# Performance work log

Hardware: AMD Instinct MI355X
Metric: run time of the kernel (lower is better)

The kernel has to match this reference:

```python
import jax, jax.numpy as jnp
import numpy as np

D_MODEL = 1024
N_HEADS = 16
HEAD_DIM = D_MODEL // N_HEADS
B, S = 2, 2048


def setup_inputs() -> dict:
    key = jax.random.key(0)
    ks = jax.random.split(key, 10)
    q = jax.random.normal(ks[0], (B, S, D_MODEL), dtype=jnp.float32)
    k = jax.random.normal(ks[1], (B, S, D_MODEL), dtype=jnp.float32)
    v = jax.random.normal(ks[2], (B, S, D_MODEL), dtype=jnp.float32)
    # causal mask: 1 where attention is forbidden (upper triangle), 0 elsewhere
    mask = jnp.triu(jnp.ones((S, S), dtype=jnp.float32), k=1)[None, None, :, :]
    scale = 0.02
    Wk = jax.random.normal(ks[3], (D_MODEL, D_MODEL), dtype=jnp.float32) * scale
    bk = jnp.zeros((D_MODEL,), dtype=jnp.float32)
    Wv = jax.random.normal(ks[4], (D_MODEL, D_MODEL), dtype=jnp.float32) * scale
    bv = jnp.zeros((D_MODEL,), dtype=jnp.float32)
    Wo = jax.random.normal(ks[5], (D_MODEL, D_MODEL), dtype=jnp.float32) * scale
    bo = jnp.zeros((D_MODEL,), dtype=jnp.float32)
    return {"query": q, "key": k, "value": v, "mask": mask,
            "Wk": Wk, "bk": bk, "Wv": Wv, "bv": bv, "Wo": Wo, "bo": bo}


def reference(query, key, value, mask, Wk, bk, Wv, bv, Wo, bo):
    b, s, d = query.shape
    h, dh = N_HEADS, HEAD_DIM

    def split(x):  # [b, s, d] -> [b, h, s, dh]
        return x.reshape(b, -1, h, dh).transpose(0, 2, 1, 3)

    # NOTE: faithful to source bug — query is projected with weights_key.
    q = split(query @ Wk.T + bk)
    k = split(key @ Wk.T + bk)
    v = split(value @ Wv.T + bv)

    inv_sqrt_dh = jnp.float32(1.0 / np.sqrt(dh))
    scores = jnp.einsum('bhqd,bhkd->bhqk', q, k) * inv_sqrt_dh
    scores = scores + mask * jnp.float32(-1e9)
    w = jax.nn.softmax(scores, axis=-1)           # [b, h, s, s]
    ctx = jnp.einsum('bhqk,bhkd->bhqd', w, v)     # [b, h, s, dh]
    concat = ctx.transpose(0, 2, 1, 3).reshape(b, -1, d)
    out = concat @ Wo.T + bo
    return (out, w)
```

## Files before the change

kernel.cpp:

```cpp
#include <hip/hip_runtime.h>
#include <stdint.h>

#define BB 2
#define SS 2048
#define DD 1024
#define HH 16
#define DH 64
#define MM 4096

typedef unsigned short u16;
typedef __attribute__((ext_vector_type(8))) __bf16 bf16x8;
typedef __attribute__((ext_vector_type(4))) float f32x4;

__device__ __forceinline__ u16 f2bf(float f) {
    union { float f; unsigned int u; } x; x.f = f;
    unsigned int u = x.u;
    return (u16)((u + 0x7fffu + ((u >> 16) & 1u)) >> 16);
}

__device__ __forceinline__ void gl_lds16(const u16* g, u16* l) {
    __builtin_amdgcn_global_load_lds(
        (const __attribute__((address_space(1))) unsigned int*)g,
        (__attribute__((address_space(3))) unsigned int*)l, 16, 0, 0);
}

__global__ __launch_bounds__(256) void cvt_kernel(const float* __restrict__ src,
                                                  u16* __restrict__ dst, int n4) {
    int i = blockIdx.x * 256 + threadIdx.x;
    if (i < n4) {
        float4 v = ((const float4*)src)[i];
        ushort4 o;
        o.x = f2bf(v.x); o.y = f2bf(v.y); o.z = f2bf(v.z); o.w = f2bf(v.w);
        ((ushort4*)dst)[i] = o;
    }
}

template <int OUT_MODE>
__device__ __forceinline__ void gemm_core(u16* As, u16* Bs,
                                          const u16* __restrict__ A,
                                          const u16* __restrict__ W,
                                          const float* __restrict__ bias,
                                          void* __restrict__ Cout,
                                          int bx, int by) {
    const int tid = threadIdx.x;
    const int lane = tid & 63, wid = tid >> 6;
    const int wy = wid >> 1, wx = wid & 1;
    const int quad = lane >> 4, cl = lane & 15;
    const int m0 = by * 128, n0 = bx * 128;

    f32x4 acc[4][4];
#pragma unroll
    for (int i = 0; i < 4; ++i)
#pragma unroll
        for (int j = 0; j < 4; ++j) acc[i][j] = (f32x4){0.f, 0.f, 0.f, 0.f};

    const int ch0 = tid;
    const int row0 = ch0 >> 2, ko0 = (ch0 & 3) * 8;
    const int ch1 = 256 + tid;
    const int row1 = ch1 >> 2, ko1 = (ch1 & 3) * 8;
    const int lb0 = (wid * 64) * 8;
    const int lb1 = (256 + wid * 64) * 8;

    for (int kt = 0; kt < 1024; kt += 32) {
        __syncthreads();
        gl_lds16(A + (size_t)(m0 + row0) * 1024 + kt + ko0, As + lb0);
        gl_lds16(W + (size_t)(n0 + row0) * 1024 + kt + ko0, Bs + lb0);
        gl_lds16(A + (size_t)(m0 + row1) * 1024 + kt + ko1, As + lb1);
        gl_lds16(W + (size_t)(n0 + row1) * 1024 + kt + ko1, Bs + lb1);
        __syncthreads();
        bf16x8 af[4], bfr[4];
#pragma unroll
        for (int t = 0; t < 4; ++t) {
            af[t]  = *(const bf16x8*)(As + (wy * 64 + t * 16 + cl) * 32 + quad * 8);
            bfr[t] = *(const bf16x8*)(Bs + (wx * 64 + t * 16 + cl) * 32 + quad * 8);
        }
#pragma unroll
        for (int mt = 0; mt < 4; ++mt)
#pragma unroll
            for (int nt = 0; nt < 4; ++nt)
                acc[mt][nt] = __builtin_amdgcn_mfma_f32_16x16x32_bf16(
                    af[mt], bfr[nt], acc[mt][nt], 0, 0, 0);
    }

#pragma unroll
    for (int mt = 0; mt < 4; ++mt) {
#pragma unroll
        for (int nt = 0; nt < 4; ++nt) {
            int n = n0 + wx * 64 + nt * 16 + cl;
            float bv = bias[n];
#pragma unroll
            for (int r = 0; r < 4; ++r) {
                int m = m0 + wy * 64 + mt * 16 + quad * 4 + r;
                float v = acc[mt][nt][r] + bv;
                if (OUT_MODE == 0) {
                    int b = m >> 11, s = m & 2047, h = n >> 6, d = n & 63;
                    ((u16*)Cout)[((size_t)(b * 16 + h) * 2048 + s) * 64 + d] = f2bf(v);
                } else if (OUT_MODE == 1) {
                    int b = m >> 11, s = m & 2047, h = n >> 6, d = n & 63;
                    ((u16*)Cout)[((size_t)(b * 16 + h) * 64 + d) * 2048 + s] = f2bf(v);
                } else {
                    ((float*)Cout)[(size_t)m * 1024 + n] = v;
                }
            }
        }
    }
}

__global__ __launch_bounds__(256, 2) void proj_kernel(
    const u16* __restrict__ Xq, const u16* __restrict__ Xk, const u16* __restrict__ Xv,
    const u16* __restrict__ Wkb, const u16* __restrict__ Wvb,
    const float* __restrict__ bk, const float* __restrict__ bv,
    u16* __restrict__ Qh, u16* __restrict__ Kh, u16* __restrict__ Vt) {
    __shared__ u16 As[128 * 32];
    __shared__ u16 Bs[128 * 32];
    int z = blockIdx.z;
    const u16* A = (z == 0) ? Xq : (z == 1) ? Xk : Xv;
    const u16* W = (z == 2) ? Wvb : Wkb;
    const float* bias = (z == 2) ? bv : bk;
    if (z == 2)
        gemm_core<1>(As, Bs, A, W, bias, Vt, blockIdx.x, blockIdx.y);
    else
        gemm_core<0>(As, Bs, A, W, bias, (z == 0) ? (void*)Qh : (void*)Kh,
                     blockIdx.x, blockIdx.y);
}

__global__ __launch_bounds__(256, 2) void outproj_kernel(
    const u16* __restrict__ Ctx, const u16* __restrict__ Wob,
    const float* __restrict__ bo, float* __restrict__ out) {
    __shared__ u16 As[128 * 32];
    __shared__ u16 Bs[128 * 32];
    gemm_core<2>(As, Bs, Ctx, Wob, bo, out, blockIdx.x, blockIdx.y);
}

__global__ __launch_bounds__(256, 2) void attn_kernel(
    const u16* __restrict__ Qh, const u16* __restrict__ Kh, const u16* __restrict__ Vt,
    float* __restrict__ Wout, u16* __restrict__ Ctx) {
    __shared__ u16 Ks[64 * 72];
    __shared__ u16 Vs[64 * 72];
    __shared__ u16 Ps[128 * 72];

    const int tid = threadIdx.x;
    const int lane = tid & 63, wid = tid >> 6;
    const int quad = lane >> 4, cl = lane & 15;
    const int bh = blockIdx.y;
    const int qb = ((bh >> 4) & 1) ? (15 - (int)blockIdx.x) : (int)blockIdx.x;
    const int q0 = qb * 128;
    const int b = bh >> 4, h = bh & 15;

    const u16* Qp = Qh + (size_t)bh * 2048 * 64;
    const u16* Kp = Kh + (size_t)bh * 2048 * 64;
    const u16* Vp = Vt + (size_t)bh * 64 * 2048;
    float* Wp = Wout + (size_t)bh * 2048 * 2048;

    bf16x8 qf[2][2];
#pragma unroll
    for (int mt = 0; mt < 2; ++mt)
#pragma unroll
        for (int ks = 0; ks < 2; ++ks) {
            int row = q0 + wid * 32 + mt * 16 + cl;
            qf[mt][ks] = *(const bf16x8*)(Qp + (size_t)row * 64 + ks * 32 + quad * 8);
        }

    float mrun[8], lrun[8];
#pragma unroll
    for (int i = 0; i < 8; ++i) { mrun[i] = -1e30f; lrun[i] = 0.f; }

    const int nkt = 2 * qb + 2;

    for (int kt = 0; kt < nkt; ++kt) {
        __syncthreads();
#pragma unroll
        for (int j = 0; j < 2; ++j) {
            int ch = j * 256 + tid;
            int row = ch >> 3, ko = (ch & 7) * 8;
            *(uint4*)(Ks + row * 72 + ko) =
                *(const uint4*)(Kp + (size_t)(kt * 64 + row) * 64 + ko);
        }
        __syncthreads();

        const bool tile_masked = (kt >= 2 * qb);
        f32x4 sc[2][4];
#pragma unroll
        for (int nt = 0; nt < 4; ++nt) {
            bf16x8 kf0 = *(const bf16x8*)(Ks + (nt * 16 + cl) * 72 + quad * 8);
            bf16x8 kf1 = *(const bf16x8*)(Ks + (nt * 16 + cl) * 72 + 32 + quad * 8);
#pragma unroll
            for (int mt = 0; mt < 2; ++mt) {
                f32x4 a = (f32x4){0.f, 0.f, 0.f, 0.f};
                a = __builtin_amdgcn_mfma_f32_16x16x32_bf16(qf[mt][0], kf0, a, 0, 0, 0);
                a = __builtin_amdgcn_mfma_f32_16x16x32_bf16(qf[mt][1], kf1, a, 0, 0, 0);
                sc[mt][nt] = a;
            }
        }
#pragma unroll
        for (int mt = 0; mt < 2; ++mt)
#pragma unroll
            for (int r = 0; r < 4; ++r) {
                int li = mt * 4 + r;
                int grow = q0 + wid * 32 + mt * 16 + quad * 4 + r;
                float tmax = -1e30f;
#pragma unroll
                for (int nt = 0; nt < 4; ++nt) {
                    int gcol = kt * 64 + nt * 16 + cl;
                    float s = sc[mt][nt][r] * 0.125f;
                    if (tile_masked) s = (gcol <= grow) ? s : -1e30f;
                    sc[mt][nt][r] = s;
                    tmax = fmaxf(tmax, s);
                }
#pragma unroll
                for (int off = 1; off < 16; off <<= 1)
                    tmax = fmaxf(tmax, __shfl_xor(tmax, off));
                float mnew = fmaxf(mrun[li], tmax);
                float sum = 0.f;
#pragma unroll
                for (int nt = 0; nt < 4; ++nt)
                    sum += __expf(sc[mt][nt][r] - mnew);
#pragma unroll
                for (int off = 1; off < 16; off <<= 1)
                    sum += __shfl_xor(sum, off);
                lrun[li] = lrun[li] * __expf(mrun[li] - mnew) + sum;
                mrun[li] = mnew;
            }
    }

    float rli[8];
#pragma unroll
    for (int i = 0; i < 8; ++i) rli[i] = 1.0f / lrun[i];

    f32x4 ctx[2][4];
#pragma unroll
    for (int mt = 0; mt < 2; ++mt)
#pragma unroll
        for (int d = 0; d < 4; ++d) ctx[mt][d] = (f32x4){0.f, 0.f, 0.f, 0.f};

    for (int kt = 0; kt < nkt; ++kt) {
        __syncthreads();
#pragma unroll
        for (int j = 0; j < 2; ++j) {
            int ch = j * 256 + tid;
            int row = ch >> 3, ko = (ch & 7) * 8;
            *(uint4*)(Ks + row * 72 + ko) =
                *(const uint4*)(Kp + (size_t)(kt * 64 + row) * 64 + ko);
            *(uint4*)(Vs + row * 72 + ko) =
                *(const uint4*)(Vp + (size_t)row * 2048 + kt * 64 + ko);
        }
        __syncthreads();

        const bool tile_masked = (kt >= 2 * qb);
        f32x4 sc[2][4];
#pragma unroll
        for (int nt = 0; nt < 4; ++nt) {
            bf16x8 kf0 = *(const bf16x8*)(Ks + (nt * 16 + cl) * 72 + quad * 8);
            bf16x8 kf1 = *(const bf16x8*)(Ks + (nt * 16 + cl) * 72 + 32 + quad * 8);
#pragma unroll
            for (int mt = 0; mt < 2; ++mt) {
                f32x4 a = (f32x4){0.f, 0.f, 0.f, 0.f};
                a = __builtin_amdgcn_mfma_f32_16x16x32_bf16(qf[mt][0], kf0, a, 0, 0, 0);
                a = __builtin_amdgcn_mfma_f32_16x16x32_bf16(qf[mt][1], kf1, a, 0, 0, 0);
                sc[mt][nt] = a;
            }
        }
#pragma unroll
        for (int mt = 0; mt < 2; ++mt)
#pragma unroll
            for (int r = 0; r < 4; ++r) {
                int li = mt * 4 + r;
                int lrow = wid * 32 + mt * 16 + quad * 4 + r;
                int grow = q0 + lrow;
                float mm = mrun[li], rl = rli[li];
#pragma unroll
                for (int nt = 0; nt < 4; ++nt) {
                    int gcol = kt * 64 + nt * 16 + cl;
                    float s = sc[mt][nt][r] * 0.125f;
                    if (tile_masked) s = (gcol <= grow) ? s : -1e30f;
                    float p = __expf(s - mm);
                    __builtin_nontemporal_store(p * rl, Wp + (size_t)grow * 2048 + gcol);
                    Ps[lrow * 72 + nt * 16 + cl] = f2bf(p);
                }
            }
        asm volatile("s_waitcnt lgkmcnt(0)" ::: "memory");

#pragma unroll
        for (int ks = 0; ks < 2; ++ks) {
            bf16x8 pf[2];
#pragma unroll
            for (int mt = 0; mt < 2; ++mt)
                pf[mt] = *(const bf16x8*)(Ps + (wid * 32 + mt * 16 + cl) * 72 + ks * 32 + quad * 8);
#pragma unroll
            for (int d = 0; d < 4; ++d) {
                bf16x8 vf = *(const bf16x8*)(Vs + (d * 16 + cl) * 72 + ks * 32 + quad * 8);
#pragma unroll
                for (int mt = 0; mt < 2; ++mt)
                    ctx[mt][d] = __builtin_amdgcn_mfma_f32_16x16x32_bf16(
                        pf[mt], vf, ctx[mt][d], 0, 0, 0);
            }
        }
    }

    for (int zt = qb + 1; zt < 16; ++zt) {
        f32x4 z = (f32x4){0.f, 0.f, 0.f, 0.f};
#pragma unroll
        for (int j = 0; j < 16; ++j) {
            int idx = j * 256 + tid;
            int row = idx >> 5, col4 = idx & 31;
            __builtin_nontemporal_store(
                z, (f32x4*)(Wp + (size_t)(q0 + row) * 2048 + zt * 128 + col4 * 4));
        }
    }

#pragma unroll
    for (int mt = 0; mt < 2; ++mt)
#pragma unroll
        for (int d = 0; d < 4; ++d)
#pragma unroll
            for (int r = 0; r < 4; ++r) {
                int li = mt * 4 + r;
                int grow = q0 + wid * 32 + mt * 16 + quad * 4 + r;
                int col = d * 16 + cl;
                float v = ctx[mt][d][r] * rli[li];
                Ctx[((size_t)(b * 2048 + grow)) * 1024 + h * 64 + col] = f2bf(v);
            }
}

extern "C" void kernel_launch(void* const* d_in, const int* in_sizes, int n_in,
                              void* d_out, int out_size, void* d_ws, size_t ws_size,
                              hipStream_t stream) {
    const float* qin = (const float*)d_in[0];
    const float* kin = (const float*)d_in[1];
    const float* vin = (const float*)d_in[2];
    const float* Wk = (const float*)d_in[4];
    const float* bk = (const float*)d_in[5];
    const float* Wv = (const float*)d_in[6];
    const float* bv = (const float*)d_in[7];
    const float* Wo = (const float*)d_in[8];
    const float* bo = (const float*)d_in[9];

    float* outp = (float*)d_out;
    float* wout = outp + (size_t)MM * DD;

    u16* Xq  = (u16*)d_ws;
    u16* Xk  = Xq  + (size_t)MM * DD;
    u16* Xv  = Xk  + (size_t)MM * DD;
    u16* Wkb = Xv  + (size_t)MM * DD;
    u16* Wvb = Wkb + (size_t)DD * DD;
    u16* Wob = Wvb + (size_t)DD * DD;
    u16* Qh  = Wob + (size_t)DD * DD;
    u16* Kh  = Qh  + (size_t)MM * DD;
    u16* Vt  = Kh  + (size_t)MM * DD;
    u16* Ctx = Vt  + (size_t)MM * DD;

    dim3 blk(256, 1, 1);
    cvt_kernel<<<dim3(MM * DD / 4 / 256, 1, 1), blk, 0, stream>>>(qin, Xq, MM * DD / 4);
    cvt_kernel<<<dim3(MM * DD / 4 / 256, 1, 1), blk, 0, stream>>>(kin, Xk, MM * DD / 4);
    cvt_kernel<<<dim3(MM * DD / 4 / 256, 1, 1), blk, 0, stream>>>(vin, Xv, MM * DD / 4);
    cvt_kernel<<<dim3(DD * DD / 4 / 256, 1, 1), blk, 0, stream>>>(Wk, Wkb, DD * DD / 4);
    cvt_kernel<<<dim3(DD * DD / 4 / 256, 1, 1), blk, 0, stream>>>(Wv, Wvb, DD * DD / 4);
    cvt_kernel<<<dim3(DD * DD / 4 / 256, 1, 1), blk, 0, stream>>>(Wo, Wob, DD * DD / 4);

    proj_kernel<<<dim3(8, 32, 3), blk, 0, stream>>>(Xq, Xk, Xv, Wkb, Wvb, bk, bv, Qh, Kh, Vt);
    attn_kernel<<<dim3(16, 32, 1), blk, 0, stream>>>(Qh, Kh, Vt, wout, Ctx);
    outproj_kernel<<<dim3(8, 32, 1), blk, 0, stream>>>(Ctx, Wob, bo, outp);
}
```

Baseline: 762.3 us.

## Drop max-subtraction in softmax, stage weight stores via LDS, fuse conversions

Removes running-max tracking and its cross-lane shuffles from softmax by exponentiating raw scaled scores and only summing, with the row-sum reduction deferred to the end of the first pass. The attention-weight output is now written as coalesced float4 nontemporal stores read back from the bf16 P tile in LDS, replacing scattered scalar stores. Six conversion launches are merged into one. Without max subtraction, large scores can overflow exp, and the stored weights carry bf16 precision instead of fp32.

```diff
diff --git a/kernel.cpp b/kernel.cpp
--- a/kernel.cpp
+++ b/kernel.cpp
@@ -18,21 +18,34 @@
     return (u16)((u + 0x7fffu + ((u >> 16) & 1u)) >> 16);
 }
 
+__device__ __forceinline__ float bf2f(u16 u) {
+    union { unsigned int u; float f; } x; x.u = ((unsigned int)u) << 16;
+    return x.f;
+}
+
 __device__ __forceinline__ void gl_lds16(const u16* g, u16* l) {
     __builtin_amdgcn_global_load_lds(
         (const __attribute__((address_space(1))) unsigned int*)g,
         (__attribute__((address_space(3))) unsigned int*)l, 16, 0, 0);
 }
 
-__global__ __launch_bounds__(256) void cvt_kernel(const float* __restrict__ src,
-                                                  u16* __restrict__ dst, int n4) {
+__global__ __launch_bounds__(256) void cvt_all_kernel(
+    const float* __restrict__ q, const float* __restrict__ k, const float* __restrict__ v,
+    const float* __restrict__ wk, const float* __restrict__ wv, const float* __restrict__ wo,
+    u16* __restrict__ Xq, u16* __restrict__ Xk, u16* __restrict__ Xv,
+    u16* __restrict__ Wkb, u16* __restrict__ Wvb, u16* __restrict__ Wob) {
     int i = blockIdx.x * 256 + threadIdx.x;
-    if (i < n4) {
-        float4 v = ((const float4*)src)[i];
-        ushort4 o;
-        o.x = f2bf(v.x); o.y = f2bf(v.y); o.z = f2bf(v.z); o.w = f2bf(v.w);
-        ((ushort4*)dst)[i] = o;
-    }
+    const float* s; u16* d; int off;
+    if (i < 1048576)      { s = q;  d = Xq;  off = i; }
+    else if (i < 2097152) { s = k;  d = Xk;  off = i - 1048576; }
+    else if (i < 3145728) { s = v;  d = Xv;  off = i - 2097152; }
+    else if (i < 3407872) { s = wk; d = Wkb; off = i - 3145728; }
+    else if (i < 3670016) { s = wv; d = Wvb; off = i - 3407872; }
+    else                  { s = wo; d = Wob; off = i - 3670016; }
+    float4 val = ((const float4*)s)[off];
+    ushort4 o;
+    o.x = f2bf(val.x); o.y = f2bf(val.y); o.z = f2bf(val.z); o.w = f2bf(val.w);
+    ((ushort4*)d)[off] = o;
 }
 
 template <int OUT_MODE>
@@ -138,6 +151,7 @@
     __shared__ u16 Ks[64 * 72];
     __shared__ u16 Vs[64 * 72];
     __shared__ u16 Ps[128 * 72];
+    __shared__ float rlS[128];
 
     const int tid = threadIdx.x;
     const int lane = tid & 63, wid = tid >> 6;
@@ -161,9 +175,9 @@
             qf[mt][ks] = *(const bf16x8*)(Qp + (size_t)row * 64 + ks * 32 + quad * 8);
         }
 
-    float mrun[8], lrun[8];
-#pragma unroll
-    for (int i = 0; i < 8; ++i) { mrun[i] = -1e30f; lrun[i] = 0.f; }
+    float lsum[8];
+#pragma unroll
+    for (int i = 0; i < 8; ++i) lsum[i] = 0.f;
 
     const int nkt = 2 * qb + 2;
 
@@ -198,34 +212,33 @@
             for (int r = 0; r < 4; ++r) {
                 int li = mt * 4 + r;
                 int grow = q0 + wid * 32 + mt * 16 + quad * 4 + r;
-                float tmax = -1e30f;
+                float acc = 0.f;
 #pragma unroll
                 for (int nt = 0; nt < 4; ++nt) {
                     int gcol = kt * 64 + nt * 16 + cl;
-                    float s = sc[mt][nt][r] * 0.125f;
-                    if (tile_masked) s = (gcol <= grow) ? s : -1e30f;
-                    sc[mt][nt][r] = s;
-                    tmax = fmaxf(tmax, s);
+                    float p = __expf(sc[mt][nt][r] * 0.125f);
+                    if (tile_masked) p = (gcol <= grow) ? p : 0.f;
+                    acc += p;
                 }
-#pragma unroll
-                for (int off = 1; off < 16; off <<= 1)
-                    tmax = fmaxf(tmax, __shfl_xor(tmax, off));
-                float mnew = fmaxf(mrun[li], tmax);
-                float sum = 0.f;
-#pragma unroll
-                for (int nt = 0; nt < 4; ++nt)
-                    sum += __expf(sc[mt][nt][r] - mnew);
-#pragma unroll
-                for (int off = 1; off < 16; off <<= 1)
-                    sum += __shfl_xor(sum, off);
-                lrun[li] = lrun[li] * __expf(mrun[li] - mnew) + sum;
-                mrun[li] = mnew;
+                lsum[li] += acc;
             }
     }
 
     float rli[8];
 #pragma unroll
-    for (int i = 0; i < 8; ++i) rli[i] = 1.0f / lrun[i];
+    for (int i = 0; i < 8; ++i) {
+        float s = lsum[i];
+#pragma unroll
+        for (int off = 1; off < 16; off <<= 1) s += __shfl_xor(s, off);
+        rli[i] = 1.0f / s;
+    }
+    if (cl == 0) {
+#pragma unroll
+        for (int mt = 0; mt < 2; ++mt)
+#pragma unroll
+            for (int r = 0; r < 4; ++r)
+                rlS[wid * 32 + mt * 16 + quad * 4 + r] = rli[mt * 4 + r];
+    }
 
     f32x4 ctx[2][4];
 #pragma unroll
@@ -264,21 +277,30 @@
         for (int mt = 0; mt < 2; ++mt)
 #pragma unroll
             for (int r = 0; r < 4; ++r) {
-                int li = mt * 4 + r;
                 int lrow = wid * 32 + mt * 16 + quad * 4 + r;
                 int grow = q0 + lrow;
-                float mm = mrun[li], rl = rli[li];
 #pragma unroll
                 for (int nt = 0; nt < 4; ++nt) {
                     int gcol = kt * 64 + nt * 16 + cl;
-                    float s = sc[mt][nt][r] * 0.125f;
-                    if (tile_masked) s = (gcol <= grow) ? s : -1e30f;
-                    float p = __expf(s - mm);
-                    __builtin_nontemporal_store(p * rl, Wp + (size_t)grow * 2048 + gcol);
+                    float p = __expf(sc[mt][nt][r] * 0.125f);
+                    if (tile_masked) p = (gcol <= grow) ? p : 0.f;
                     Ps[lrow * 72 + nt * 16 + cl] = f2bf(p);
                 }
             }
-        asm volatile("s_waitcnt lgkmcnt(0)" ::: "memory");
+        __syncthreads();
+
+#pragma unroll
+        for (int c = 0; c < 8; ++c) {
+            int idx = c * 256 + tid;
+            int row = idx >> 4, q4 = idx & 15;
+            const u16* pw = Ps + row * 72 + q4 * 4;
+            float rl = rlS[row];
+            f32x4 o;
+            o[0] = bf2f(pw[0]) * rl; o[1] = bf2f(pw[1]) * rl;
+            o[2] = bf2f(pw[2]) * rl; o[3] = bf2f(pw[3]) * rl;
+            __builtin_nontemporal_store(
+                o, (f32x4*)(Wp + (size_t)(q0 + row) * 2048 + kt * 64 + q4 * 4));
+        }
 
 #pragma unroll
         for (int ks = 0; ks < 2; ++ks) {
@@ -350,13 +372,8 @@
     u16* Ctx = Vt  + (size_t)MM * DD;
 
     dim3 blk(256, 1, 1);
-    cvt_kernel<<<dim3(MM * DD / 4 / 256, 1, 1), blk, 0, stream>>>(qin, Xq, MM * DD / 4);
-    cvt_kernel<<<dim3(MM * DD / 4 / 256, 1, 1), blk, 0, stream>>>(kin, Xk, MM * DD / 4);
-    cvt_kernel<<<dim3(MM * DD / 4 / 256, 1, 1), blk, 0, stream>>>(vin, Xv, MM * DD / 4);
-    cvt_kernel<<<dim3(DD * DD / 4 / 256, 1, 1), blk, 0, stream>>>(Wk, Wkb, DD * DD / 4);
-    cvt_kernel<<<dim3(DD * DD / 4 / 256, 1, 1), blk, 0, stream>>>(Wv, Wvb, DD * DD / 4);
-    cvt_kernel<<<dim3(DD * DD / 4 / 256, 1, 1), blk, 0, stream>>>(Wo, Wob, DD * DD / 4);
-
+    cvt_all_kernel<<<dim3(15360, 1, 1), blk, 0, stream>>>(
+        qin, kin, vin, Wk, Wv, Wo, Xq, Xk, Xv, Wkb, Wvb, Wob);
     proj_kernel<<<dim3(8, 32, 3), blk, 0, stream>>>(Xq, Xk, Xv, Wkb, Wvb, bk, bv, Qh, Kh, Vt);
     attn_kernel<<<dim3(16, 32, 1), blk, 0, stream>>>(Qh, Kh, Vt, wout, Ctx);
     outproj_kernel<<<dim3(8, 32, 1), blk, 0, stream>>>(Ctx, Wob, bo, outp);
```

Result: faster. 739.3 us (-3.0%).
